# Optimization experiments

Hardware: AMD Instinct MI355X
Metric: run time of the kernel (lower is better)

The kernel has to match this reference:

```python
import jax, jax.numpy as jnp
import numpy as np

B = 4096; NINP = 512; NHID = 2048
NBI = 1; NBO = 8; TOPK = 4; NMRI = 2
BSO = NHID // NBO           # 256 (block_size_out)
ATT_OUT = BSO * 4           # 1024
GRU_NINP = ATT_OUT * NBO    # 8192
BSI = GRU_NINP // NBO       # 1024 (GRU per-block input size)
DK_I = 64                   # inp_att d_k (n_head=1)
NH_M = 4; DK_M = 16; DV_M = 16  # mha heads/dims


def setup_inputs() -> dict:
    key = jax.random.key(0)
    ks = jax.random.split(key, 16)
    r = lambda i, shape, s=0.01: (s * jax.random.normal(ks[i], shape)).astype(jnp.float32)
    return {
        "inp": jax.random.normal(ks[0], (B, NBI * NINP), dtype=jnp.float32),
        "hx": jax.random.normal(ks[1], (B, NHID), dtype=jnp.float32),
        "cx": jax.random.normal(ks[2], (B, NHID), dtype=jnp.float32),
        "step": 0,
        # inp_att (GroupLinear q over NBO blocks; k,v over NMRI write slots; fc out)
        "Wq_i": r(3, (NBO, BSO, DK_I)),
        "Wk_i": r(4, (NMRI, NINP, DK_I)),
        "Wv_i": r(5, (NMRI, NINP, ATT_OUT)),
        "fc_i_w": r(6, (ATT_OUT, ATT_OUT), 0.02),
        "fc_i_b": jnp.zeros((ATT_OUT,), jnp.float32),
        # mha (communication attention among blocks)
        "Wq_m": r(7, (NBO, BSO, NH_M * DK_M)),
        "Wk_m": r(8, (NBO, BSO, NH_M * DK_M)),
        "Wv_m": r(9, (NBO, BSO, NH_M * DV_M)),
        "fc_m_w": r(10, (NH_M * DV_M, BSO), 0.05),
        "fc_m_b": jnp.zeros((BSO,), jnp.float32),
        "gate_m_w": r(11, (NH_M * DV_M, BSO), 0.05),
        "gate_m_b": jnp.zeros((BSO,), jnp.float32),
        # block-diagonal GRU cell (blockified params: only diagonal blocks kept)
        "Wih": r(12, (NBO, 3 * BSO, BSI), 0.02),
        "Whh": r(13, (NBO, 3 * BSO, BSO), 0.02),
        "bih": jnp.zeros((NBO, 3 * BSO), jnp.float32),
        "bhh": jnp.zeros((NBO, 3 * BSO), jnp.float32),
    }


def _forward(inp, hx, cx, Wq_i, Wk_i, Wv_i, fc_i_w, fc_i_b, Wq_m, Wk_m, Wv_m,
             fc_m_w, fc_m_b, gate_m_w, gate_m_b, Wih, Whh, bih, bhh):
    b = inp.shape[0]
    # --- build read slots: slot 0 = zeros (null), slot 1 = input ---
    x = inp.reshape(b, NBI, NINP)
    x = jnp.tile(x, (1, NMRI - 1, 1))
    x = jnp.concatenate([jnp.zeros_like(x[:, :1]), x], axis=1)            # (b, NMRI, ninp)
    hx3 = hx.reshape(b, NBO, BSO)
    # --- inp_att: n_head=1, residual=False (gate_fc unused); Sparse_attention no-op (topk>=len_k) ---
    q = jnp.einsum('bni,nio->bno', hx3, Wq_i)                             # (b, NBO, DK_I)
    k = jnp.einsum('bni,nio->bno', x, Wk_i)                               # (b, NMRI, DK_I)
    v = jnp.einsum('bni,nio->bno', x, Wv_i)                               # (b, NMRI, ATT_OUT)
    iatt = jax.nn.softmax(jnp.einsum('bqd,bkd->bqk', q, k) / float(np.sqrt(DK_I)), axis=-1)
    inp_use = jnp.einsum('bqk,bkv->bqv', iatt, v)                         # (b, NBO, ATT_OUT)
    inp_use = (inp_use @ fc_i_w + fc_i_b).reshape(b, NBO * ATT_OUT)
    # --- top-k block mask: zero out the (NBO-TOPK) blocks most attentive to the null slot ---
    drop_idx = jax.lax.top_k(iatt[:, :, 0], NBO - TOPK)[1]                # (b, NBO-TOPK)
    mask = jnp.ones((b, NBO), inp.dtype).at[jnp.arange(b)[:, None], drop_idx].set(0.0)
    mask = jax.lax.stop_gradient(mask)                                    # mask.detach()
    mask_w = jnp.repeat(mask[:, :, None], BSO, axis=2).reshape(b, NHID)
    # --- block-diagonal GRUCell: h' = (1-z)*n + z*h ---
    x3 = inp_use.reshape(b, NBO, BSI)
    gx = jnp.einsum('bki,koi->bko', x3, Wih) + bih                        # (b, NBO, 3*BSO)
    gh = jnp.einsum('bkj,koj->bko', hx3, Whh) + bhh
    xr, xz, xn = jnp.split(gx, 3, axis=-1)
    hr, hz, hn = jnp.split(gh, 3, axis=-1)
    r = jax.nn.sigmoid(xr + hr)
    z = jax.nn.sigmoid(xz + hz)
    n = jnp.tanh(xn + r * hn)
    h_new = (1.0 - z) * n + z * hx3                                       # (b, NBO, BSO)
    # --- step attention among blocks; blocked_grad = identity fwd, grad*mask bwd ---
    m3 = mask[:, :, None]
    hg = m3 * h_new + jax.lax.stop_gradient((1.0 - m3) * h_new)
    qm = jnp.einsum('bni,nio->bno', hg, Wq_m).reshape(b, NBO, NH_M, DK_M)
    km = jnp.einsum('bni,nio->bno', hg, Wk_m).reshape(b, NBO, NH_M, DK_M)
    vm = jnp.einsum('bni,nio->bno', hg, Wv_m).reshape(b, NBO, NH_M, DV_M)
    am = jax.nn.softmax(jnp.einsum('bqhd,bkhd->bhqk', qm, km) / float(np.sqrt(DK_M)), axis=-1)
    om = jnp.einsum('bhqk,bkhd->bqhd', am, vm).reshape(b, NBO, NH_M * DV_M)
    att = jax.nn.sigmoid(om @ gate_m_w + gate_m_b) * jnp.tanh(om @ fc_m_w + fc_m_b)  # residual=True gating
    h_new = (h_new + att).reshape(b, NHID)
    # --- gated state update (GRU: cx_new = hx_new) ---
    hx_out = mask_w * h_new + (1.0 - mask_w) * hx
    cx_out = mask_w * h_new + (1.0 - mask_w) * cx
    return hx_out, cx_out, mask_w


def reference(inp, hx, cx, step, Wq_i, Wk_i, Wv_i, fc_i_w, fc_i_b, Wq_m, Wk_m, Wv_m,
              fc_m_w, fc_m_b, gate_m_w, gate_m_b, Wih, Whh, bih, bhh):
    del step  # unused by the math
    return _forward(inp, hx, cx, Wq_i, Wk_i, Wv_i, fc_i_w, fc_i_b, Wq_m, Wk_m, Wv_m,
                    fc_m_w, fc_m_b, gate_m_w, gate_m_b, Wih, Whh, bih, bhh)
```

## Files before the change

kernel.cpp:

```cpp
#include <hip/hip_runtime.h>
#include <hip/hip_bf16.h>

#define B_SZ 4096
#define NHID_ 2048

typedef __bf16 bf16x8 __attribute__((ext_vector_type(8)));
typedef float f32x4 __attribute__((ext_vector_type(4)));

__device__ __forceinline__ float sigmoidf_(float x) { return 1.f / (1.f + expf(-x)); }
__device__ __forceinline__ float b2f_(unsigned short u) {
    unsigned v = (unsigned)u << 16;
    return __builtin_bit_cast(float, v);
}

#define GLDS16(gp, lp) __builtin_amdgcn_global_load_lds( \
    (const __attribute__((address_space(1))) void*)(gp), \
    (__attribute__((address_space(3))) void*)(lp), 16, 0, 0)

__global__ __launch_bounds__(256) void f2b3_kernel(
    const float* __restrict__ s0, __hip_bfloat16* __restrict__ d0,
    const float* __restrict__ s1, __hip_bfloat16* __restrict__ d1,
    const float* __restrict__ s2, __hip_bfloat16* __restrict__ d2)
{
    long i = (long)blockIdx.x * 256 + threadIdx.x;
    const float* src; __hip_bfloat16* dst; long off;
    if (i < 524288)       { src = s0; dst = d0; off = i; }
    else if (i < 917504)  { src = s1; dst = d1; off = i - 524288; }
    else                  { src = s2; dst = d2; off = i - 917504; }
    float4 v = ((const float4*)src)[off];
    __hip_bfloat16 b0 = __float2bfloat16(v.x);
    __hip_bfloat16 b1 = __float2bfloat16(v.y);
    __hip_bfloat16 b2 = __float2bfloat16(v.z);
    __hip_bfloat16 b3 = __float2bfloat16(v.w);
    ushort4 u;
    u.x = *(unsigned short*)&b0; u.y = *(unsigned short*)&b1;
    u.z = *(unsigned short*)&b2; u.w = *(unsigned short*)&b3;
    ((ushort4*)dst)[off] = u;
}

__global__ __launch_bounds__(256) void wih_prep(
    const float* __restrict__ Wih, const float* __restrict__ fc_i_b,
    const float* __restrict__ bih, __hip_bfloat16* __restrict__ Wihb,
    float* __restrict__ cb)
{
    long j = blockIdx.x;
    const float* row = Wih + j * 1024;
    __hip_bfloat16* drow = Wihb + j * 1024;
    int i = threadIdx.x * 4;
    float4 v = *(const float4*)(row + i);
    __hip_bfloat16 b0 = __float2bfloat16(v.x);
    __hip_bfloat16 b1 = __float2bfloat16(v.y);
    __hip_bfloat16 b2 = __float2bfloat16(v.z);
    __hip_bfloat16 b3 = __float2bfloat16(v.w);
    ushort4 u;
    u.x = *(unsigned short*)&b0; u.y = *(unsigned short*)&b1;
    u.z = *(unsigned short*)&b2; u.w = *(unsigned short*)&b3;
    *(ushort4*)(drow + i) = u;
    float s = fc_i_b[i] * v.x + fc_i_b[i + 1] * v.y +
              fc_i_b[i + 2] * v.z + fc_i_b[i + 3] * v.w;
#pragma unroll
    for (int off = 32; off > 0; off >>= 1) s += __shfl_xor(s, off, 64);
    __shared__ float red[4];
    if ((threadIdx.x & 63) == 0) red[threadIdx.x >> 6] = s;
    __syncthreads();
    if (threadIdx.x == 0) cb[j] = red[0] + red[1] + red[2] + red[3] + bih[j];
}

__global__ __launch_bounds__(256) void tconv_kernel(
    const float* __restrict__ src, int C, long sS,
    __hip_bfloat16* __restrict__ dst, int ldd, long sD)
{
    src += (long)blockIdx.z * sS;
    dst += (long)blockIdx.z * sD;
    const int r0 = blockIdx.y * 32, c0 = blockIdx.x * 32;
    const int tx = threadIdx.x & 31, ty = threadIdx.x >> 5;
    __shared__ float tile[32][33];
#pragma unroll
    for (int i = 0; i < 4; ++i)
        tile[ty + i * 8][tx] = src[(long)(r0 + ty + i * 8) * C + c0 + tx];
    __syncthreads();
#pragma unroll
    for (int i = 0; i < 4; ++i)
        dst[(long)(c0 + ty + i * 8) * ldd + r0 + tx] = __float2bfloat16(tile[tx][ty + i * 8]);
}

__global__ __launch_bounds__(256) void tconv_wm(
    const float* __restrict__ Wq, const float* __restrict__ Wk,
    const float* __restrict__ Wv, __hip_bfloat16* __restrict__ WmT)
{
    const int z = blockIdx.z;
    const int which = z >> 3, nb = z & 7;
    const float* src = (which == 0) ? Wq : (which == 1) ? Wk : Wv;
    src += (long)nb * 16384;
    __hip_bfloat16* dst = WmT + (long)nb * 49152 + which * 64 * 256;
    const int r0 = blockIdx.y * 32, c0 = blockIdx.x * 32;
    const int tx = threadIdx.x & 31, ty = threadIdx.x >> 5;
    __shared__ float tile[32][33];
#pragma unroll
    for (int i = 0; i < 4; ++i)
        tile[ty + i * 8][tx] = src[(long)(r0 + ty + i * 8) * 64 + c0 + tx];
    __syncthreads();
#pragma unroll
    for (int i = 0; i < 4; ++i)
        dst[(long)(c0 + ty + i * 8) * 256 + r0 + tx] = __float2bfloat16(tile[tx][ty + i * 8]);
}

__global__ __launch_bounds__(256) void fcg_prep(
    const float* __restrict__ fc_w, const float* __restrict__ gate_w,
    __hip_bfloat16* __restrict__ fcgT)
{
    int tid = blockIdx.x * 256 + threadIdx.x;
    int np = tid >> 6, k = tid & 63;
    int o = (np >> 5) * 16 + (np & 15);
    const float* src = ((np >> 4) & 1) ? gate_w : fc_w;
    fcgT[tid] = __float2bfloat16(src[k * 256 + o]);
}

#define GM_BM 64
#define GM_BN 64
#define GM_BK 16

__global__ __launch_bounds__(256) void gemm_nn(
    const float* __restrict__ A, const float* __restrict__ Bm, float* __restrict__ C,
    int M, int N, int K, int lda, int ldb, int ldc,
    long sA, long sB, long sC)
{
    const int z = blockIdx.z;
    A += (long)z * sA; Bm += (long)z * sB; C += (long)z * sC;
    const int m0 = blockIdx.y * GM_BM;
    const int n0 = blockIdx.x * GM_BN;
    const int tid = threadIdx.x;
    const int tx = tid & 15;
    const int ty = tid >> 4;

    __shared__ float As[GM_BK][GM_BM + 4];
    __shared__ float Bs[GM_BK][GM_BN + 4];

    float acc[4][4] = {};

    for (int k0 = 0; k0 < K; k0 += GM_BK) {
#pragma unroll
        for (int i = 0; i < 4; ++i) {
            int idx = tid + i * 256;
            int r = idx >> 4, c = idx & 15;
            As[c][r] = A[(long)(m0 + r) * lda + k0 + c];
        }
#pragma unroll
        for (int i = 0; i < 4; ++i) {
            int idx = tid + i * 256;
            int r = idx >> 6, c = idx & 63;
            Bs[r][c] = Bm[(long)(k0 + r) * ldb + n0 + c];
        }
        __syncthreads();
#pragma unroll
        for (int kk = 0; kk < GM_BK; ++kk) {
            float4 a4 = *(const float4*)&As[kk][ty * 4];
            float4 b4 = *(const float4*)&Bs[kk][tx * 4];
            float av[4] = {a4.x, a4.y, a4.z, a4.w};
            float bv[4] = {b4.x, b4.y, b4.z, b4.w};
#pragma unroll
            for (int i = 0; i < 4; ++i)
#pragma unroll
                for (int j = 0; j < 4; ++j)
                    acc[i][j] += av[i] * bv[j];
        }
        __syncthreads();
    }
#pragma unroll
    for (int i = 0; i < 4; ++i) {
        long m = m0 + ty * 4 + i;
#pragma unroll
        for (int j = 0; j < 4; ++j) {
            int n = n0 + tx * 4 + j;
            C[m * ldc + n] = acc[i][j];
        }
    }
}

__global__ __launch_bounds__(256) void gemm_nt_f32(
    const float* __restrict__ A, int lda,
    const float* __restrict__ BT, int ldb,
    float* __restrict__ C, int ldc, int K, long sB, long sC)
{
    BT += (long)blockIdx.z * sB;
    C  += (long)blockIdx.z * sC;
    const int m0 = blockIdx.y * 64;
    const int n0 = blockIdx.x * 64;
    const int tid = threadIdx.x;
    const int tx = tid & 15;
    const int ty = tid >> 4;

    __shared__ float As[16][68];
    __shared__ float Bs[64][17];

    float acc[4][4] = {};

    for (int k0 = 0; k0 < K; k0 += 16) {
#pragma unroll
        for (int i = 0; i < 4; ++i) {
            int idx = tid + i * 256;
            int r = idx >> 4, c = idx & 15;
            As[c][r] = A[(long)(m0 + r) * lda + k0 + c];
        }
#pragma unroll
        for (int i = 0; i < 4; ++i) {
            int idx = tid + i * 256;
            int r = idx >> 4, c = idx & 15;
            Bs[r][c] = BT[(long)(n0 + r) * ldb + k0 + c];
        }
        __syncthreads();
#pragma unroll
        for (int kk = 0; kk < 16; ++kk) {
            float4 a4 = *(const float4*)&As[kk][ty * 4];
            float av[4] = {a4.x, a4.y, a4.z, a4.w};
            float bv[4];
#pragma unroll
            for (int j = 0; j < 4; ++j) bv[j] = Bs[tx * 4 + j][kk];
#pragma unroll
            for (int i = 0; i < 4; ++i)
#pragma unroll
                for (int j = 0; j < 4; ++j)
                    acc[i][j] += av[i] * bv[j];
        }
        __syncthreads();
    }
#pragma unroll
    for (int i = 0; i < 4; ++i) {
        long m = m0 + ty * 4 + i;
#pragma unroll
        for (int j = 0; j < 4; ++j) {
            int n = n0 + tx * 4 + j;
            C[m * ldc + n] = acc[i][j];
        }
    }
}

__global__ __launch_bounds__(256) void s1_mask_fused(
    const float* __restrict__ hx,
    const float* __restrict__ p,
    float* __restrict__ a_buf, float* __restrict__ mask_buf,
    __hip_bfloat16* __restrict__ hxb)
{
    const int wave = threadIdx.x >> 6;
    const int lane = threadIdx.x & 63;
    const long b = (long)blockIdx.x * 4 + wave;
    const long base = b * 2048 + lane * 4;
    float s1v[8];
#pragma unroll
    for (int n = 0; n < 8; ++n) {
        float4 hv = *(const float4*)(hx + base + n * 256);
        float4 pv = *(const float4*)(p + base + n * 256);
        __hip_bfloat16 c0 = __float2bfloat16(hv.x);
        __hip_bfloat16 c1 = __float2bfloat16(hv.y);
        __hip_bfloat16 c2 = __float2bfloat16(hv.z);
        __hip_bfloat16 c3 = __float2bfloat16(hv.w);
        ushort4 u;
        u.x = *(unsigned short*)&c0; u.y = *(unsigned short*)&c1;
        u.z = *(unsigned short*)&c2; u.w = *(unsigned short*)&c3;
        *(ushort4*)(hxb + base + n * 256) = u;
        float s = hv.x * pv.x + hv.y * pv.y + hv.z * pv.z + hv.w * pv.w;
#pragma unroll
        for (int off = 32; off > 0; off >>= 1) s += __shfl_xor(s, off, 64);
        s1v[n] = s * 0.125f;
    }
    unsigned maskbits = 0;
#pragma unroll
    for (int n = 0; n < 8; ++n) {
        int rank = 0;
#pragma unroll
        for (int m = 0; m < 8; ++m) {
            if (m == n) continue;
            if (s1v[m] < s1v[n] || (s1v[m] == s1v[n] && m < n)) rank++;
        }
        if (rank >= 4) maskbits |= (1u << n);
    }
    if (lane < 8) {
        float sv = s1v[0];
#pragma unroll
        for (int n = 1; n < 8; ++n)
            if (lane == n) sv = s1v[n];
        a_buf[b * 8 + lane] = sigmoidf_(sv);
        mask_buf[b * 8 + lane] = ((maskbits >> lane) & 1u) ? 1.0f : 0.0f;
    }
}

__global__ __launch_bounds__(256) void gemm_mfma_obf16(
    const __hip_bfloat16* __restrict__ A, int lda,
    const __hip_bfloat16* __restrict__ BT, int ldb,
    __hip_bfloat16* __restrict__ C, int ldc, int K)
{
    const int m0 = blockIdx.y * 128;
    const int n0 = blockIdx.x * 64;
    const int tid = threadIdx.x;
    const int lane = tid & 63, wid = tid >> 6;
    const int wr = wid >> 1, wc = wid & 1;
    const int l15 = lane & 15, l4 = lane >> 4;

    __shared__ __align__(16) char lds_raw[16384 + 8192];
    char* Alds = lds_raw;
    char* Blds = lds_raw + 16384;

    f32x4 acc[4][2] = {};

    for (int k0 = 0; k0 < K; k0 += 64) {
#pragma unroll
        for (int ii = 0; ii < 4; ++ii) {
            int issue = ii * 4 + wid;
            int chunk = issue * 64 + lane;
            int r = chunk >> 3, cs = chunk & 7;
            int cl = cs ^ (r & 7);
            const __hip_bfloat16* g = A + (long)(m0 + r) * lda + k0 + cl * 8;
            GLDS16(g, Alds + issue * 1024);
        }
#pragma unroll
        for (int jj = 0; jj < 2; ++jj) {
            int issue = jj * 4 + wid;
            int chunk = issue * 64 + lane;
            int r = chunk >> 3, cs = chunk & 7;
            int cl = cs ^ (r & 7);
            const __hip_bfloat16* g = BT + (long)(n0 + r) * ldb + k0 + cl * 8;
            GLDS16(g, Blds + issue * 1024);
        }
        __syncthreads();
#pragma unroll
        for (int kk = 0; kk < 2; ++kk) {
            bf16x8 af[4], bfr[2];
#pragma unroll
            for (int im = 0; im < 4; ++im) {
                int r = wr * 64 + im * 16 + l15;
                int cl = (kk * 4 + l4) ^ (l15 & 7);
                af[im] = *(const bf16x8*)(Alds + r * 128 + cl * 16);
            }
#pragma unroll
            for (int jn = 0; jn < 2; ++jn) {
                int r = wc * 32 + jn * 16 + l15;
                int cl = (kk * 4 + l4) ^ (l15 & 7);
                bfr[jn] = *(const bf16x8*)(Blds + r * 128 + cl * 16);
            }
#pragma unroll
            for (int im = 0; im < 4; ++im)
#pragma unroll
                for (int jn = 0; jn < 2; ++jn)
                    acc[im][jn] = __builtin_amdgcn_mfma_f32_16x16x32_bf16(
                        af[im], bfr[jn], acc[im][jn], 0, 0, 0);
        }
        __syncthreads();
    }
#pragma unroll
    for (int im = 0; im < 4; ++im)
#pragma unroll
        for (int reg = 0; reg < 4; ++reg) {
            long m = m0 + wr * 64 + im * 16 + l4 * 4 + reg;
#pragma unroll
            for (int jn = 0; jn < 2; ++jn) {
                int n = n0 + wc * 32 + jn * 16 + l15;
                C[m * ldc + n] = __float2bfloat16(acc[im][jn][reg]);
            }
        }
}

__global__ __launch_bounds__(256) void gemm_mfma_qkv(
    const __hip_bfloat16* __restrict__ hnewb,
    const __hip_bfloat16* __restrict__ WmT,
    __hip_bfloat16* __restrict__ qout)
{
    const int z = blockIdx.z;
    const int m0 = blockIdx.y * 128;
    const int n0 = blockIdx.x * 64;
    const int tid = threadIdx.x;
    const int lane = tid & 63, wid = tid >> 6;
    const int wr = wid >> 1, wc = wid & 1;
    const int l15 = lane & 15, l4 = lane >> 4;

    const __hip_bfloat16* A = hnewb + z * 256;
    const __hip_bfloat16* BT = WmT + (long)z * 192 * 256;

    __shared__ __align__(16) char lds_raw[16384 + 8192];
    char* Alds = lds_raw;
    char* Blds = lds_raw + 16384;

    f32x4 acc[4][2] = {};

    for (int k0 = 0; k0 < 256; k0 += 64) {
#pragma unroll
        for (int ii = 0; ii < 4; ++ii) {
            int issue = ii * 4 + wid;
            int chunk = issue * 64 + lane;
            int r = chunk >> 3, cs = chunk & 7;
            int cl = cs ^ (r & 7);
            const __hip_bfloat16* g = A + (long)(m0 + r) * 2048 + k0 + cl * 8;
            GLDS16(g, Alds + issue * 1024);
        }
#pragma unroll
        for (int jj = 0; jj < 2; ++jj) {
            int issue = jj * 4 + wid;
            int chunk = issue * 64 + lane;
            int r = chunk >> 3, cs = chunk & 7;
            int cl = cs ^ (r & 7);
            const __hip_bfloat16* g = BT + (long)(n0 + r) * 256 + k0 + cl * 8;
            GLDS16(g, Blds + issue * 1024);
        }
        __syncthreads();
#pragma unroll
        for (int kk = 0; kk < 2; ++kk) {
            bf16x8 af[4], bfr[2];
#pragma unroll
            for (int im = 0; im < 4; ++im) {
                int r = wr * 64 + im * 16 + l15;
                int cl = (kk * 4 + l4) ^ (l15 & 7);
                af[im] = *(const bf16x8*)(Alds + r * 128 + cl * 16);
            }
#pragma unroll
            for (int jn = 0; jn < 2; ++jn) {
                int r = wc * 32 + jn * 16 + l15;
                int cl = (kk * 4 + l4) ^ (l15 & 7);
                bfr[jn] = *(const bf16x8*)(Blds + r * 128 + cl * 16);
            }
#pragma unroll
            for (int im = 0; im < 4; ++im)
#pragma unroll
                for (int jn = 0; jn < 2; ++jn)
                    acc[im][jn] = __builtin_amdgcn_mfma_f32_16x16x32_bf16(
                        af[im], bfr[jn], acc[im][jn], 0, 0, 0);
        }
        __syncthreads();
    }
#pragma unroll
    for (int jn = 0; jn < 2; ++jn) {
        int j = n0 + wc * 32 + jn * 16 + l15;
        int g = j >> 6, d = j & 63;
        __hip_bfloat16* outp = qout + (long)g * 2097152 + (long)z * 64 + d;
#pragma unroll
        for (int im = 0; im < 4; ++im)
#pragma unroll
            for (int reg = 0; reg < 4; ++reg) {
                long m = m0 + wr * 64 + im * 16 + l4 * 4 + reg;
                outp[m * 512] = __float2bfloat16(acc[im][jn][reg]);
            }
    }
}

__global__ __launch_bounds__(512) void gru_fused_mfma(
    const __hip_bfloat16* __restrict__ wfcb,
    const __hip_bfloat16* __restrict__ hxb,
    const float* __restrict__ a_buf,
    const float* __restrict__ cb,
    const __hip_bfloat16* __restrict__ Wihb,
    const __hip_bfloat16* __restrict__ Whhb,
    const float* __restrict__ bhh,
    __hip_bfloat16* __restrict__ hnewb)
{
    const int bid = blockIdx.x;
    const int kblk = bid & 7;
    const int r_ = bid >> 3;
    const int ol0 = (r_ & 7) * 32;
    const int m0 = (r_ >> 3) * 128;
    const int tid = threadIdx.x;
    const int lane = tid & 63, wid = tid >> 6;
    const int wr = wid >> 1;
    const int wc = wid & 1;
    const int l15 = lane & 15, l4 = lane >> 4;

    __shared__ __align__(16) char lds_raw[2 * 28672];

    f32x4 accx[2][3] = {};
    f32x4 acch[2][3] = {};

    const __hip_bfloat16* Wk = Wihb + (long)kblk * 768 * 1024;
    const __hip_bfloat16* Wh = Whhb + (long)kblk * 768 * 256;
    const __hip_bfloat16* hxk = hxb + kblk * 256;

    const int iiA0 = wid, iiA1 = wid + 8;
    const int cA0 = iiA0 * 64 + lane, rA0 = cA0 >> 3, clA0 = (cA0 & 7) ^ (rA0 & 7);
    const int cA1 = iiA1 * 64 + lane, rA1 = cA1 >> 3, clA1 = (cA1 & 7) ^ (rA1 & 7);
    const int jjB0 = wid, jjB1 = wid + 8;
    const int cB0 = jjB0 * 64 + lane, rB0 = cB0 >> 3, clB0 = (cB0 & 7) ^ (rB0 & 7);
    const int cB1 = jjB1 * 64 + lane, rB1 = cB1 >> 3, clB1 = (cB1 & 7) ^ (rB1 & 7);
    const bool hasB1 = (wid < 4);
    const int gg0 = rB0 >> 5, oll0 = rB0 & 31;
    const int gg1 = (rB1 >> 5) & 3, oll1 = rB1 & 31;
    const int dA0 = iiA0 * 1024, dA1 = iiA1 * 1024;
    const int dB0 = 16384 + jjB0 * 1024, dB1 = 16384 + jjB1 * 1024;

    const __hip_bfloat16* pA0 = wfcb + (long)(m0 + rA0) * 1024 + clA0 * 8;
    const __hip_bfloat16* pA1 = wfcb + (long)(m0 + rA1) * 1024 + clA1 * 8;
    const __hip_bfloat16* pB0 = Wk + (long)(gg0 * 256 + ol0 + oll0) * 1024 + clB0 * 8;
    const __hip_bfloat16* pB1 = Wk + (long)(gg1 * 256 + ol0 + oll1) * 1024 + clB1 * 8;

#define STAGE4(buf) do {                                                       \
    char* L = lds_raw + (buf) * 28672;                                         \
    GLDS16(pA0, L + dA0);                                                      \
    GLDS16(pA1, L + dA1);                                                      \
    GLDS16(pB0, L + dB0);                                                      \
    if (hasB1) GLDS16(pB1, L + dB1);                                           \
    pA0 += 64; pA1 += 64; pB0 += 64; pB1 += 64;                                \
} while (0)

    int offA[2][2], offB[2][3];
#pragma unroll
    for (int kk = 0; kk < 2; ++kk) {
        int cl = (kk * 4 + l4) ^ (l15 & 7);
#pragma unroll
        for (int im = 0; im < 2; ++im)
            offA[kk][im] = (wr * 32 + im * 16 + l15) * 128 + cl * 16;
#pragma unroll
        for (int g = 0; g < 3; ++g)
            offB[kk][g] = 16384 + (g * 32 + wc * 16 + l15) * 128 + cl * 16;
    }

#define COMPUTE(acc, buf) do {                                                 \
    char* L = lds_raw + (buf) * 28672;                                         \
    _Pragma("unroll") for (int kk = 0; kk < 2; ++kk) {                         \
        bf16x8 af[2], bfr[3];                                                  \
        _Pragma("unroll") for (int im = 0; im < 2; ++im)                       \
            af[im] = *(const bf16x8*)(L + offA[kk][im]);                       \
        _Pragma("unroll") for (int g = 0; g < 3; ++g)                          \
            bfr[g] = *(const bf16x8*)(L + offB[kk][g]);                        \
        _Pragma("unroll") for (int im = 0; im < 2; ++im)                       \
            _Pragma("unroll") for (int g = 0; g < 3; ++g)                      \
                acc[im][g] = __builtin_amdgcn_mfma_f32_16x16x32_bf16(          \
                    af[im], bfr[g], acc[im][g], 0, 0, 0);                      \
    }                                                                          \
} while (0)

    STAGE4(0);
    asm volatile("s_waitcnt vmcnt(0)" ::: "memory");
    __syncthreads();

    int cur = 0;
    for (int t = 0; t < 16; ++t) {
        if (t < 15) {
            STAGE4(cur ^ 1);
        } else {
            pA0 = hxk + (long)(m0 + rA0) * 2048 + clA0 * 8;
            pA1 = hxk + (long)(m0 + rA1) * 2048 + clA1 * 8;
            pB0 = Wh + (long)(gg0 * 256 + ol0 + oll0) * 256 + clB0 * 8;
            pB1 = Wh + (long)(gg1 * 256 + ol0 + oll1) * 256 + clB1 * 8;
            STAGE4(cur ^ 1);
        }
        __builtin_amdgcn_s_setprio(1);
        COMPUTE(accx, cur);
        __builtin_amdgcn_s_setprio(0);
        asm volatile("s_waitcnt vmcnt(0)" ::: "memory");
        __syncthreads();
        cur ^= 1;
    }
    for (int t = 0; t < 4; ++t) {
        if (t < 3) STAGE4(cur ^ 1);
        __builtin_amdgcn_s_setprio(1);
        COMPUTE(acch, cur);
        __builtin_amdgcn_s_setprio(0);
        asm volatile("s_waitcnt vmcnt(0)" ::: "memory");
        __syncthreads();
        cur ^= 1;
    }
#undef STAGE4
#undef COMPUTE

    const int ol = ol0 + wc * 16 + l15;
    const float* cbk = cb + kblk * 768;
    const float cb0 = cbk[ol], cb1 = cbk[256 + ol], cb2 = cbk[512 + ol];
    const float* bhk = bhh + kblk * 768;
    const float bh0 = bhk[ol], bh1 = bhk[256 + ol], bh2 = bhk[512 + ol];
#pragma unroll
    for (int im = 0; im < 2; ++im) {
#pragma unroll
        for (int reg = 0; reg < 4; ++reg) {
            long m = m0 + wr * 32 + im * 16 + l4 * 4 + reg;
            float av = a_buf[m * 8 + kblk];
            float gx0 = av * accx[im][0][reg] + cb0;
            float gx1 = av * accx[im][1][reg] + cb1;
            float gx2 = av * accx[im][2][reg] + cb2;
            float gh0 = acch[im][0][reg] + bh0;
            float gh1 = acch[im][1][reg] + bh1;
            float gh2 = acch[im][2][reg] + bh2;
            float rr = sigmoidf_(gx0 + gh0);
            float zz = sigmoidf_(gx1 + gh1);
            float nn = tanhf(gx2 + rr * gh2);
            long idx = m * 2048 + kblk * 256 + ol;
            float hxv = __bfloat162float(hxb[idx]);
            hnewb[idx] = __float2bfloat16((1.f - zz) * nn + zz * hxv);
        }
    }
}

__global__ __launch_bounds__(256) void mattn_kernel(
    const __hip_bfloat16* __restrict__ qm, const __hip_bfloat16* __restrict__ km,
    const __hip_bfloat16* __restrict__ vm, __hip_bfloat16* __restrict__ omb)
{
    const int t = threadIdx.x;
    const int local = t & 31;
    const long b = (long)blockIdx.x * 8 + (t >> 5);
    const int h = local >> 3, qn = local & 7;
    const long base = b * 512 + h * 16;

    float qv[16];
#pragma unroll
    for (int i = 0; i < 2; ++i) {
        bf16x8 v = *(const bf16x8*)(qm + base + qn * 64 + i * 8);
#pragma unroll
        for (int j = 0; j < 8; ++j) qv[i * 8 + j] = (float)v[j];
    }
    float sc[8];
#pragma unroll
    for (int kn = 0; kn < 8; ++kn) {
        float s = 0.f;
#pragma unroll
        for (int i = 0; i < 2; ++i) {
            bf16x8 v = *(const bf16x8*)(km + base + kn * 64 + i * 8);
#pragma unroll
            for (int j = 0; j < 8; ++j) s += qv[i * 8 + j] * (float)v[j];
        }
        sc[kn] = s * 0.25f;
    }
    float mx = sc[0];
#pragma unroll
    for (int kn = 1; kn < 8; ++kn) mx = fmaxf(mx, sc[kn]);
    float ssum = 0.f;
#pragma unroll
    for (int kn = 0; kn < 8; ++kn) { sc[kn] = expf(sc[kn] - mx); ssum += sc[kn]; }
    float inv = 1.f / ssum;

    float acc[16] = {};
#pragma unroll
    for (int kn = 0; kn < 8; ++kn) {
        float w = sc[kn] * inv;
#pragma unroll
        for (int i = 0; i < 2; ++i) {
            bf16x8 v = *(const bf16x8*)(vm + base + kn * 64 + i * 8);
#pragma unroll
            for (int j = 0; j < 8; ++j) acc[i * 8 + j] += w * (float)v[j];
        }
    }
#pragma unroll
    for (int i = 0; i < 2; ++i) {
        bf16x8 o;
#pragma unroll
        for (int j = 0; j < 8; ++j) o[j] = (__bf16)acc[i * 8 + j];
        *(bf16x8*)(omb + base + qn * 64 + i * 8) = o;
    }
}

__global__ __launch_bounds__(256) void att_final(
    const __hip_bfloat16* __restrict__ omb,
    const __hip_bfloat16* __restrict__ fcgT,
    const float* __restrict__ fc_b, const float* __restrict__ gate_b,
    const __hip_bfloat16* __restrict__ hnewb,
    const float* __restrict__ maskb,
    const float* __restrict__ hx, const float* __restrict__ cx,
    float* __restrict__ hx_out, float* __restrict__ cx_out,
    float* __restrict__ mask_w)
{
    const int m0 = blockIdx.y * 128;
    const int n0 = blockIdx.x * 64;
    const int tid = threadIdx.x;
    const int lane = tid & 63, wid = tid >> 6;
    const int wr = wid >> 1, wc = wid & 1;
    const int l15 = lane & 15, l4 = lane >> 4;

    __shared__ __align__(16) char lds_raw[16384 + 8192];
    char* Alds = lds_raw;
    char* Blds = lds_raw + 16384;

    f32x4 acc[4][2] = {};
#pragma unroll
    for (int ii = 0; ii < 4; ++ii) {
        int issue = ii * 4 + wid;
        int chunk = issue * 64 + lane;
        int r = chunk >> 3, cs = chunk & 7;
        int cl = cs ^ (r & 7);
        const __hip_bfloat16* g = omb + (long)(m0 + r) * 64 + cl * 8;
        GLDS16(g, Alds + issue * 1024);
    }
#pragma unroll
    for (int jj = 0; jj < 2; ++jj) {
        int issue = jj * 4 + wid;
        int chunk = issue * 64 + lane;
        int r = chunk >> 3, cs = chunk & 7;
        int cl = cs ^ (r & 7);
        const __hip_bfloat16* g = fcgT + (long)(n0 + r) * 64 + cl * 8;
        GLDS16(g, Blds + issue * 1024);
    }
    __syncthreads();
#pragma unroll
    for (int kk = 0; kk < 2; ++kk) {
        bf16x8 af[4], bfr[2];
#pragma unroll
        for (int im = 0; im < 4; ++im) {
            int r = wr * 64 + im * 16 + l15;
            int cl = (kk * 4 + l4) ^ (l15 & 7);
            af[im] = *(const bf16x8*)(Alds + r * 128 + cl * 16);
        }
#pragma unroll
        for (int jn = 0; jn < 2; ++jn) {
            int r = wc * 32 + jn * 16 + l15;
            int cl = (kk * 4 + l4) ^ (l15 & 7);
            bfr[jn] = *(const bf16x8*)(Blds + r * 128 + cl * 16);
        }
#pragma unroll
        for (int im = 0; im < 4; ++im)
#pragma unroll
            for (int jn = 0; jn < 2; ++jn)
                acc[im][jn] = __builtin_amdgcn_mfma_f32_16x16x32_bf16(
                    af[im], bfr[jn], acc[im][jn], 0, 0, 0);
    }
    const int o = ((n0 + wc * 32) >> 1) + l15;
    const float fb = fc_b[o], gb = gate_b[o];
#pragma unroll
    for (int im = 0; im < 4; ++im)
#pragma unroll
        for (int reg = 0; reg < 4; ++reg) {
            long m = m0 + wr * 64 + im * 16 + l4 * 4 + reg;
            long idx = m * 256 + o;
            float mv = maskb[m];
            float att = sigmoidf_(acc[im][1][reg] + gb) * tanhf(acc[im][0][reg] + fb);
            float ho, co;
            if (mv != 0.f) {
                float h2 = __bfloat162float(hnewb[idx]) + att;
                ho = h2; co = h2;
            } else {
                ho = hx[idx]; co = cx[idx];
            }
            hx_out[idx] = ho;
            cx_out[idx] = co;
            mask_w[idx] = mv;
        }
}

extern "C" void kernel_launch(void* const* d_in, const int* in_sizes, int n_in,
                              void* d_out, int out_size, void* d_ws, size_t ws_size,
                              hipStream_t stream)
{
    const float* inp     = (const float*)d_in[0];
    const float* hx      = (const float*)d_in[1];
    const float* cx      = (const float*)d_in[2];
    const float* Wq_i    = (const float*)d_in[4];
    const float* Wk_i    = (const float*)d_in[5];
    const float* Wv_i    = (const float*)d_in[6];
    const float* fc_i_w  = (const float*)d_in[7];
    const float* fc_i_b  = (const float*)d_in[8];
    const float* Wq_m    = (const float*)d_in[9];
    const float* Wk_m    = (const float*)d_in[10];
    const float* Wv_m    = (const float*)d_in[11];
    const float* fc_m_w  = (const float*)d_in[12];
    const float* fc_m_b  = (const float*)d_in[13];
    const float* gate_m_w= (const float*)d_in[14];
    const float* gate_m_b= (const float*)d_in[15];
    const float* Wih     = (const float*)d_in[16];
    const float* Whh     = (const float*)d_in[17];
    const float* bih     = (const float*)d_in[18];
    const float* bhh     = (const float*)d_in[19];

    float* out = (float*)d_out;
    const long BH = (long)B_SZ * NHID_;
    float* hx_out = out;
    float* cx_out = out + BH;
    float* mask_w = out + 2 * BH;
    __hip_bfloat16* hxb = (__hip_bfloat16*)out;
    __hip_bfloat16* qkvb = (__hip_bfloat16*)out;
    float* pbuf = cx_out;

    float* w = (float*)d_ws;
    float* a_buf = w;
    float* maskb = w + 32768;
    float* cbuf  = w + 65536;
    __hip_bfloat16* fcgT = (__hip_bfloat16*)(w + 73728);
    __hip_bfloat16* WmT  = (__hip_bfloat16*)(w + 90112);
    __hip_bfloat16* Wihb = (__hip_bfloat16*)(w + 286720);
    __hip_bfloat16* Whhb = (__hip_bfloat16*)(w + 3432448);
    __hip_bfloat16* wfcb = (__hip_bfloat16*)(w + 4218880);
    __hip_bfloat16* hnewb= (__hip_bfloat16*)(w + 6316032);
    float* krow = w + 8413184;
    __hip_bfloat16* inpb = (__hip_bfloat16*)(w + 8675328);
    __hip_bfloat16* WvB  = (__hip_bfloat16*)(w + 9723904);
    __hip_bfloat16* fcT  = (__hip_bfloat16*)(w + 9986048);
    __hip_bfloat16* WvFT = (__hip_bfloat16*)(w + 10510336);
    __hip_bfloat16* omb  = (__hip_bfloat16*)(w + 286720);

    wih_prep<<<dim3(6144), dim3(256), 0, stream>>>(Wih, fc_i_b, bih, Wihb, cbuf);
    f2b3_kernel<<<dim3(4096), dim3(256), 0, stream>>>(
        inp, inpb, Whh, Whhb, Wv_i + 512 * 1024, WvB);
    tconv_kernel<<<dim3(32, 32, 1), dim3(256), 0, stream>>>(fc_i_w, 1024, 0, fcT, 1024, 0);
    tconv_wm<<<dim3(2, 8, 24), dim3(256), 0, stream>>>(Wq_m, Wk_m, Wv_m, WmT);
    fcg_prep<<<dim3(128), dim3(256), 0, stream>>>(fc_m_w, gate_m_w, fcgT);
    gemm_nn<<<dim3(1, 64, 1), dim3(256), 0, stream>>>(
        inp, Wk_i + 512 * 64, krow, 4096, 64, 512, 512, 64, 64, 0, 0, 0);
    gemm_nt_f32<<<dim3(4, 64, 8), dim3(256), 0, stream>>>(
        krow, 64, Wq_i, 64, pbuf, 2048, 64, 16384, 256);
    s1_mask_fused<<<dim3(1024), dim3(256), 0, stream>>>(hx, pbuf, a_buf, maskb, hxb);
    gemm_mfma_obf16<<<dim3(8, 8, 1), dim3(256), 0, stream>>>(
        fcT, 1024, WvB, 1024, WvFT, 512, 1024);
    gemm_mfma_obf16<<<dim3(16, 32, 1), dim3(256), 0, stream>>>(
        inpb, 512, WvFT, 512, wfcb, 1024, 512);
    gru_fused_mfma<<<dim3(2048), dim3(512), 0, stream>>>(
        wfcb, hxb, a_buf, cbuf, Wihb, Whhb, bhh, hnewb);
    gemm_mfma_qkv<<<dim3(3, 32, 8), dim3(256), 0, stream>>>(hnewb, WmT, qkvb);
    mattn_kernel<<<dim3(512), dim3(256), 0, stream>>>(
        qkvb, qkvb + 2097152, qkvb + 4194304, omb);
    att_final<<<dim3(8, 256, 1), dim3(256), 0, stream>>>(
        omb, fcgT, fc_m_b, gate_m_b, hnewb, maskb, hx, cx, hx_out, cx_out, mask_w);
}
```

Before: 262.7 us.

## Merge prep kernels into one launch and deepen GRU GEMM prefetch pipeline

Five small weight and input conversion kernels are folded into a single prep_all launch that dispatches on block index, cutting kernel launch and tail overhead. In the fused GRU MFMA kernel, the two-stage loop becomes one 20-iteration loop that keeps two stages in flight. It waits with partial vmcnt counts instead of draining all loads, and uses raw barriers with sched_barrier fences. The aim is to overlap global-to-LDS loads with MFMA compute. The risk is that the vmcnt counts, which depend on the hasB1 path, or the buffer reuse could be wrong and cause races.

```diff
diff --git a/kernel.cpp b/kernel.cpp
--- a/kernel.cpp
+++ b/kernel.cpp
@@ -8,112 +8,103 @@
 typedef float f32x4 __attribute__((ext_vector_type(4)));
 
 __device__ __forceinline__ float sigmoidf_(float x) { return 1.f / (1.f + expf(-x)); }
-__device__ __forceinline__ float b2f_(unsigned short u) {
-    unsigned v = (unsigned)u << 16;
-    return __builtin_bit_cast(float, v);
-}
 
 #define GLDS16(gp, lp) __builtin_amdgcn_global_load_lds( \
     (const __attribute__((address_space(1))) void*)(gp), \
     (__attribute__((address_space(3))) void*)(lp), 16, 0, 0)
 
-__global__ __launch_bounds__(256) void f2b3_kernel(
-    const float* __restrict__ s0, __hip_bfloat16* __restrict__ d0,
-    const float* __restrict__ s1, __hip_bfloat16* __restrict__ d1,
-    const float* __restrict__ s2, __hip_bfloat16* __restrict__ d2)
-{
-    long i = (long)blockIdx.x * 256 + threadIdx.x;
-    const float* src; __hip_bfloat16* dst; long off;
-    if (i < 524288)       { src = s0; dst = d0; off = i; }
-    else if (i < 917504)  { src = s1; dst = d1; off = i - 524288; }
-    else                  { src = s2; dst = d2; off = i - 917504; }
-    float4 v = ((const float4*)src)[off];
-    __hip_bfloat16 b0 = __float2bfloat16(v.x);
-    __hip_bfloat16 b1 = __float2bfloat16(v.y);
-    __hip_bfloat16 b2 = __float2bfloat16(v.z);
-    __hip_bfloat16 b3 = __float2bfloat16(v.w);
-    ushort4 u;
-    u.x = *(unsigned short*)&b0; u.y = *(unsigned short*)&b1;
-    u.z = *(unsigned short*)&b2; u.w = *(unsigned short*)&b3;
-    ((ushort4*)dst)[off] = u;
-}
-
-__global__ __launch_bounds__(256) void wih_prep(
+__global__ __launch_bounds__(256) void prep_all(
     const float* __restrict__ Wih, const float* __restrict__ fc_i_b,
     const float* __restrict__ bih, __hip_bfloat16* __restrict__ Wihb,
-    float* __restrict__ cb)
-{
-    long j = blockIdx.x;
-    const float* row = Wih + j * 1024;
-    __hip_bfloat16* drow = Wihb + j * 1024;
-    int i = threadIdx.x * 4;
-    float4 v = *(const float4*)(row + i);
-    __hip_bfloat16 b0 = __float2bfloat16(v.x);
-    __hip_bfloat16 b1 = __float2bfloat16(v.y);
-    __hip_bfloat16 b2 = __float2bfloat16(v.z);
-    __hip_bfloat16 b3 = __float2bfloat16(v.w);
-    ushort4 u;
-    u.x = *(unsigned short*)&b0; u.y = *(unsigned short*)&b1;
-    u.z = *(unsigned short*)&b2; u.w = *(unsigned short*)&b3;
-    *(ushort4*)(drow + i) = u;
-    float s = fc_i_b[i] * v.x + fc_i_b[i + 1] * v.y +
-              fc_i_b[i + 2] * v.z + fc_i_b[i + 3] * v.w;
-#pragma unroll
-    for (int off = 32; off > 0; off >>= 1) s += __shfl_xor(s, off, 64);
-    __shared__ float red[4];
-    if ((threadIdx.x & 63) == 0) red[threadIdx.x >> 6] = s;
-    __syncthreads();
-    if (threadIdx.x == 0) cb[j] = red[0] + red[1] + red[2] + red[3] + bih[j];
-}
-
-__global__ __launch_bounds__(256) void tconv_kernel(
-    const float* __restrict__ src, int C, long sS,
-    __hip_bfloat16* __restrict__ dst, int ldd, long sD)
-{
-    src += (long)blockIdx.z * sS;
-    dst += (long)blockIdx.z * sD;
-    const int r0 = blockIdx.y * 32, c0 = blockIdx.x * 32;
-    const int tx = threadIdx.x & 31, ty = threadIdx.x >> 5;
-    __shared__ float tile[32][33];
-#pragma unroll
-    for (int i = 0; i < 4; ++i)
-        tile[ty + i * 8][tx] = src[(long)(r0 + ty + i * 8) * C + c0 + tx];
-    __syncthreads();
-#pragma unroll
-    for (int i = 0; i < 4; ++i)
-        dst[(long)(c0 + ty + i * 8) * ldd + r0 + tx] = __float2bfloat16(tile[tx][ty + i * 8]);
-}
-
-__global__ __launch_bounds__(256) void tconv_wm(
-    const float* __restrict__ Wq, const float* __restrict__ Wk,
-    const float* __restrict__ Wv, __hip_bfloat16* __restrict__ WmT)
-{
-    const int z = blockIdx.z;
-    const int which = z >> 3, nb = z & 7;
-    const float* src = (which == 0) ? Wq : (which == 1) ? Wk : Wv;
-    src += (long)nb * 16384;
-    __hip_bfloat16* dst = WmT + (long)nb * 49152 + which * 64 * 256;
-    const int r0 = blockIdx.y * 32, c0 = blockIdx.x * 32;
-    const int tx = threadIdx.x & 31, ty = threadIdx.x >> 5;
-    __shared__ float tile[32][33];
-#pragma unroll
-    for (int i = 0; i < 4; ++i)
-        tile[ty + i * 8][tx] = src[(long)(r0 + ty + i * 8) * 64 + c0 + tx];
-    __syncthreads();
-#pragma unroll
-    for (int i = 0; i < 4; ++i)
-        dst[(long)(c0 + ty + i * 8) * 256 + r0 + tx] = __float2bfloat16(tile[tx][ty + i * 8]);
-}
-
-__global__ __launch_bounds__(256) void fcg_prep(
-    const float* __restrict__ fc_w, const float* __restrict__ gate_w,
+    float* __restrict__ cb,
+    const float* __restrict__ inp, __hip_bfloat16* __restrict__ inpb,
+    const float* __restrict__ Whh, __hip_bfloat16* __restrict__ Whhb,
+    const float* __restrict__ WvBsrc, __hip_bfloat16* __restrict__ WvB,
+    const float* __restrict__ fc_i_w, __hip_bfloat16* __restrict__ fcT,
+    const float* __restrict__ Wq_m, const float* __restrict__ Wk_m,
+    const float* __restrict__ Wv_m, __hip_bfloat16* __restrict__ WmT,
+    const float* __restrict__ fc_m_w, const float* __restrict__ gate_m_w,
     __hip_bfloat16* __restrict__ fcgT)
 {
-    int tid = blockIdx.x * 256 + threadIdx.x;
-    int np = tid >> 6, k = tid & 63;
-    int o = (np >> 5) * 16 + (np & 15);
-    const float* src = ((np >> 4) & 1) ? gate_w : fc_w;
-    fcgT[tid] = __float2bfloat16(src[k * 256 + o]);
+    __shared__ float smem[32 * 33];
+    const int bid = blockIdx.x;
+    const int tid = threadIdx.x;
+
+    if (bid < 6144) {
+        long j = bid;
+        const float* row = Wih + j * 1024;
+        __hip_bfloat16* drow = Wihb + j * 1024;
+        int i = tid * 4;
+        float4 v = *(const float4*)(row + i);
+        __hip_bfloat16 b0 = __float2bfloat16(v.x);
+        __hip_bfloat16 b1 = __float2bfloat16(v.y);
+        __hip_bfloat16 b2 = __float2bfloat16(v.z);
+        __hip_bfloat16 b3 = __float2bfloat16(v.w);
+        ushort4 u;
+        u.x = *(unsigned short*)&b0; u.y = *(unsigned short*)&b1;
+        u.z = *(unsigned short*)&b2; u.w = *(unsigned short*)&b3;
+        *(ushort4*)(drow + i) = u;
+        float s = fc_i_b[i] * v.x + fc_i_b[i + 1] * v.y +
+                  fc_i_b[i + 2] * v.z + fc_i_b[i + 3] * v.w;
+#pragma unroll
+        for (int off = 32; off > 0; off >>= 1) s += __shfl_xor(s, off, 64);
+        if ((tid & 63) == 0) smem[tid >> 6] = s;
+        __syncthreads();
+        if (tid == 0) cb[j] = smem[0] + smem[1] + smem[2] + smem[3] + bih[j];
+    } else if (bid < 10240) {
+        long i = (long)(bid - 6144) * 256 + tid;
+        const float* src; __hip_bfloat16* dst; long off;
+        if (i < 524288)       { src = inp;    dst = inpb; off = i; }
+        else if (i < 917504)  { src = Whh;    dst = Whhb; off = i - 524288; }
+        else                  { src = WvBsrc; dst = WvB;  off = i - 917504; }
+        float4 v = ((const float4*)src)[off];
+        __hip_bfloat16 b0 = __float2bfloat16(v.x);
+        __hip_bfloat16 b1 = __float2bfloat16(v.y);
+        __hip_bfloat16 b2 = __float2bfloat16(v.z);
+        __hip_bfloat16 b3 = __float2bfloat16(v.w);
+        ushort4 u;
+        u.x = *(unsigned short*)&b0; u.y = *(unsigned short*)&b1;
+        u.z = *(unsigned short*)&b2; u.w = *(unsigned short*)&b3;
+        ((ushort4*)dst)[off] = u;
+    } else if (bid < 11264) {
+        int lb = bid - 10240;
+        int r0 = (lb >> 5) * 32, c0 = (lb & 31) * 32;
+        int tx = tid & 31, ty = tid >> 5;
+        float (*tile)[33] = (float(*)[33])smem;
+#pragma unroll
+        for (int i = 0; i < 4; ++i)
+            tile[ty + i * 8][tx] = fc_i_w[(long)(r0 + ty + i * 8) * 1024 + c0 + tx];
+        __syncthreads();
+#pragma unroll
+        for (int i = 0; i < 4; ++i)
+            fcT[(long)(c0 + ty + i * 8) * 1024 + r0 + tx] =
+                __float2bfloat16(tile[tx][ty + i * 8]);
+    } else if (bid < 11648) {
+        int lb = bid - 11264;
+        int z = lb >> 4, rem = lb & 15;
+        int by = rem >> 1, bx = rem & 1;
+        int which = z >> 3, nb = z & 7;
+        const float* src = (which == 0) ? Wq_m : (which == 1) ? Wk_m : Wv_m;
+        src += (long)nb * 16384;
+        __hip_bfloat16* dst = WmT + (long)nb * 49152 + which * 64 * 256;
+        int r0 = by * 32, c0 = bx * 32;
+        int tx = tid & 31, ty = tid >> 5;
+        float (*tile)[33] = (float(*)[33])smem;
+#pragma unroll
+        for (int i = 0; i < 4; ++i)
+            tile[ty + i * 8][tx] = src[(long)(r0 + ty + i * 8) * 64 + c0 + tx];
+        __syncthreads();
+#pragma unroll
+        for (int i = 0; i < 4; ++i)
+            dst[(long)(c0 + ty + i * 8) * 256 + r0 + tx] =
+                __float2bfloat16(tile[tx][ty + i * 8]);
+    } else {
+        int t = (bid - 11648) * 256 + tid;
+        int np = t >> 6, k = t & 63;
+        int o = (np >> 5) * 16 + (np & 15);
+        const float* src = ((np >> 4) & 1) ? gate_m_w : fc_m_w;
+        fcgT[t] = __float2bfloat16(src[k * 256 + o]);
+    }
 }
 
 #define GM_BM 64
@@ -524,34 +515,30 @@
 } while (0)
 
     STAGE4(0);
-    asm volatile("s_waitcnt vmcnt(0)" ::: "memory");
-    __syncthreads();
+    STAGE4(1);
 
     int cur = 0;
-    for (int t = 0; t < 16; ++t) {
-        if (t < 15) {
-            STAGE4(cur ^ 1);
-        } else {
-            pA0 = hxk + (long)(m0 + rA0) * 2048 + clA0 * 8;
-            pA1 = hxk + (long)(m0 + rA1) * 2048 + clA1 * 8;
-            pB0 = Wh + (long)(gg0 * 256 + ol0 + oll0) * 256 + clB0 * 8;
-            pB1 = Wh + (long)(gg1 * 256 + ol0 + oll1) * 256 + clB1 * 8;
-            STAGE4(cur ^ 1);
-        }
+    for (int t = 0; t < 20; ++t) {
+        if (t == 19)      asm volatile("s_waitcnt vmcnt(0)" ::: "memory");
+        else if (hasB1)   asm volatile("s_waitcnt vmcnt(4)" ::: "memory");
+        else              asm volatile("s_waitcnt vmcnt(3)" ::: "memory");
+        __builtin_amdgcn_s_barrier();
+        __builtin_amdgcn_sched_barrier(0);
         __builtin_amdgcn_s_setprio(1);
-        COMPUTE(accx, cur);
+        if (t < 16) COMPUTE(accx, cur);
+        else        COMPUTE(acch, cur);
         __builtin_amdgcn_s_setprio(0);
-        asm volatile("s_waitcnt vmcnt(0)" ::: "memory");
-        __syncthreads();
-        cur ^= 1;
-    }
-    for (int t = 0; t < 4; ++t) {
-        if (t < 3) STAGE4(cur ^ 1);
-        __builtin_amdgcn_s_setprio(1);
-        COMPUTE(acch, cur);
-        __builtin_amdgcn_s_setprio(0);
-        asm volatile("s_waitcnt vmcnt(0)" ::: "memory");
-        __syncthreads();
+        __builtin_amdgcn_sched_barrier(0);
+        __builtin_amdgcn_s_barrier();
+        if (t < 18) {
+            if (t == 14) {
+                pA0 = hxk + (long)(m0 + rA0) * 2048 + clA0 * 8;
+                pA1 = hxk + (long)(m0 + rA1) * 2048 + clA1 * 8;
+                pB0 = Wh + (long)(gg0 * 256 + ol0 + oll0) * 256 + clB0 * 8;
+                pB1 = Wh + (long)(gg1 * 256 + ol0 + oll1) * 256 + clB1 * 8;
+            }
+            STAGE4(cur);
+        }
         cur ^= 1;
     }
 #undef STAGE4
@@ -777,12 +764,10 @@
     __hip_bfloat16* WvFT = (__hip_bfloat16*)(w + 10510336);
     __hip_bfloat16* omb  = (__hip_bfloat16*)(w + 286720);
 
-    wih_prep<<<dim3(6144), dim3(256), 0, stream>>>(Wih, fc_i_b, bih, Wihb, cbuf);
-    f2b3_kernel<<<dim3(4096), dim3(256), 0, stream>>>(
-        inp, inpb, Whh, Whhb, Wv_i + 512 * 1024, WvB);
-    tconv_kernel<<<dim3(32, 32, 1), dim3(256), 0, stream>>>(fc_i_w, 1024, 0, fcT, 1024, 0);
-    tconv_wm<<<dim3(2, 8, 24), dim3(256), 0, stream>>>(Wq_m, Wk_m, Wv_m, WmT);
-    fcg_prep<<<dim3(128), dim3(256), 0, stream>>>(fc_m_w, gate_m_w, fcgT);
+    prep_all<<<dim3(11776), dim3(256), 0, stream>>>(
+        Wih, fc_i_b, bih, Wihb, cbuf,
+        inp, inpb, Whh, Whhb, Wv_i + 512 * 1024, WvB,
+        fc_i_w, fcT, Wq_m, Wk_m, Wv_m, WmT, fc_m_w, gate_m_w, fcgT);
     gemm_nn<<<dim3(1, 64, 1), dim3(256), 0, stream>>>(
         inp, Wk_i + 512 * 64, krow, 4096, 64, 512, 512, 64, 64, 0, 0, 0);
     gemm_nt_f32<<<dim3(4, 64, 8), dim3(256), 0, stream>>>(
```

Measured after the change: 295.5 us. 1.12x slower.
